# Performance work log

Measured on AMD Instinct MI355X. Metric: run time of the kernel, lower is better.

## Reference

```python
import jax, jax.numpy as jnp
import numpy as np

EPS = 1e-8
WAITK = 9
STRIDE = 1
TARGET_STEP = 0  # module's self.target_step default (training path)
NEG_INF = -1e9


def setup_inputs() -> dict:
    key = jax.random.key(0)
    ks = jax.random.split(key, 5)
    S, B, D, E, H = 2048, 32, 1024, 1024, 1024  # src_len, bsz, dec_dim, enc_dim, energy hidden
    return {
        "input": jax.random.normal(ks[0], (B, D), jnp.float32),
        "source_hids": jax.random.normal(ks[1], (S, B, E), jnp.float32),
        "encoder_padding_mask": jnp.zeros((S, B), dtype=bool),
        "W_dec": jax.random.normal(ks[2], (D, H), jnp.float32) / np.sqrt(D).astype(np.float32),
        "W_enc": jax.random.normal(ks[3], (E, H), jnp.float32) / np.sqrt(E).astype(np.float32),
        "b": jnp.zeros((H,), jnp.float32),
        "v": jax.random.normal(ks[4], (H,), jnp.float32) / np.sqrt(H).astype(np.float32),
    }


def _softattn_energy(inp, source_hids, mask, W_dec, W_enc, b, v):
    # additive energy: v^T tanh(W_dec dec + W_enc enc + b), padding -> -inf
    dec = inp @ W_dec + b                                  # (B, H)
    enc = jnp.einsum('sbe,eh->sbh', source_hids, W_enc)    # (S, B, H)
    e = jnp.einsum('sbh,h->sb', jnp.tanh(enc + dec[None, :, :]), v)  # (S, B)
    return jnp.where(mask, NEG_INF, e)


def reference(input, source_hids, encoder_padding_mask, W_dec, W_enc, b, v):
    S, B, _ = source_hids.shape
    # get_encoder_pointer: min((target_step + waitk - 1 + 1) * stride, src_len - 1)
    ptr = min((TARGET_STEP + WAITK) * STRIDE, S - 1)

    # expected_hard_alignment: one-hot at ptr - 1
    alpha = jnp.zeros((S, B), jnp.float32).at[ptr - 1].set(1.0)

    # expected_soft_alignment: stable exp + eps, zero positions >= ptr, normalize
    e = _softattn_energy(input, source_hids, encoder_padding_mask, W_dec, W_enc, b, v)
    exp_e = jnp.exp(e - jnp.max(e, axis=0, keepdims=True)) + EPS
    keep = (jnp.arange(S) < ptr)[:, None]
    exp_e = jnp.where(keep, exp_e, 0.0)
    beta = exp_e / jnp.sum(exp_e, axis=0, keepdims=True)

    # weighted context: sum_s beta[s,b] * source_hids[s,b,:]
    output = jnp.einsum('sb,sbe->be', beta, source_hids)
    return output, alpha
```

## Files before the change

### kernel.cpp

```cpp
#include <hip/hip_runtime.h>
#include <hip/hip_bf16.h>
#include <math.h>

#define S_LEN 2048
#define B_SZ  32
#define DIM   1024
#define PTR   9
#define EPSV  1e-8f
#define NEGINF -1e9f
#define MROWS 320

typedef __attribute__((ext_vector_type(8)))  short  short8;
typedef __attribute__((ext_vector_type(16))) float  f32x16;

__device__ __forceinline__ short f2bf(float x) {
    __hip_bfloat16 h = __float2bfloat16(x);
    return *(short*)&h;
}

__device__ __forceinline__ float fast_tanh(float x) {
    float xc = fminf(fmaxf(x, -20.f), 20.f);
    float t = __expf(2.f * xc);
    return (t - 1.f) * __builtin_amdgcn_rcpf(t + 1.f);
}

__global__ __launch_bounds__(256) void k_gemm(
    const float* __restrict__ input, const float* __restrict__ src,
    const float* __restrict__ Wdec, const float* __restrict__ Wenc,
    float* __restrict__ Cp, float* __restrict__ alpha)
{
    const int nt = blockIdx.x;
    const int mt = blockIdx.y;
    const int kz = blockIdx.z;
    const float* W     = (mt == 0) ? Wdec : Wenc;
    const float* Abase = (mt == 0) ? input : (src + (size_t)(mt - 1) * B_SZ * DIM);
    const int tid = threadIdx.x;
    const int w = tid >> 6, lane = tid & 63;
    const int r32 = lane & 31, kh = lane >> 5;
    const int kbase = kz * 512 + w * 128;
    const float* Ap = Abase + (size_t)r32 * DIM + kbase + kh * 8;
    const float* Bp = W + (size_t)(kbase + kh * 8) * DIM + nt * 32 + r32;

    if (kz == 0) {
        int bidl = mt * 32 + nt;
        if (bidl < 64) {
            int f = (bidl * 256 + tid) * 4;
            float val = (f >= 256 && f < 288) ? 1.0f : 0.0f;
            float4 o = {val, val, val, val};
            *(float4*)(alpha + f) = o;
        }
    }

    f32x16 acc;
    #pragma unroll
    for (int i = 0; i < 16; i++) acc[i] = 0.f;

    #pragma unroll 4
    for (int k = 0; k < 128; k += 16) {
        float4 a0 = *(const float4*)(Ap + k);
        float4 a1 = *(const float4*)(Ap + k + 4);
        const float* bp = Bp + (size_t)k * DIM;
        float bv0 = bp[0 * DIM], bv1 = bp[1 * DIM], bv2 = bp[2 * DIM], bv3 = bp[3 * DIM];
        float bv4 = bp[4 * DIM], bv5 = bp[5 * DIM], bv6 = bp[6 * DIM], bv7 = bp[7 * DIM];
        short8 af, bf;
        af[0] = f2bf(a0.x); af[1] = f2bf(a0.y); af[2] = f2bf(a0.z); af[3] = f2bf(a0.w);
        af[4] = f2bf(a1.x); af[5] = f2bf(a1.y); af[6] = f2bf(a1.z); af[7] = f2bf(a1.w);
        bf[0] = f2bf(bv0);  bf[1] = f2bf(bv1);  bf[2] = f2bf(bv2);  bf[3] = f2bf(bv3);
        bf[4] = f2bf(bv4);  bf[5] = f2bf(bv5);  bf[6] = f2bf(bv6);  bf[7] = f2bf(bv7);
        acc = __builtin_amdgcn_mfma_f32_32x32x16_bf16(af, bf, acc, 0, 0, 0);
    }

    __shared__ float red[4 * 64 * 17];
    const int base = (w * 64 + lane) * 17;
    #pragma unroll
    for (int r = 0; r < 16; r++) red[base + r] = acc[r];
    __syncthreads();
    const int L = tid & 63, g = tid >> 6;
    const int khL = L >> 5, col = L & 31;
    float* Cz = Cp + (size_t)kz * MROWS * DIM;
    #pragma unroll
    for (int j = 0; j < 4; j++) {
        int r = g * 4 + j;
        float s = red[(0 * 64 + L) * 17 + r] + red[(1 * 64 + L) * 17 + r]
                + red[(2 * 64 + L) * 17 + r] + red[(3 * 64 + L) * 17 + r];
        int row = (r & 3) + 8 * (r >> 2) + 4 * khL;
        Cz[(size_t)(mt * 32 + row) * DIM + nt * 32 + col] = s;
    }
}

__global__ __launch_bounds__(256) void k_tail(
    const float* __restrict__ Cp,
    const unsigned char* __restrict__ mask,
    const float* __restrict__ bias, const float* __restrict__ v,
    const float* __restrict__ src, float* __restrict__ out)
{
    const int b  = blockIdx.x;
    const int hs = blockIdx.y;
    const int tid = threadIdx.x;
    const int h = tid * 4;
    const float* C0 = Cp;
    const float* C1 = Cp + (size_t)MROWS * DIM;

    const int hc = hs * 128 + (tid & 31) * 4;
    float4 sv[PTR];
    #pragma unroll
    for (int s = 0; s < PTR; s++)
        sv[s] = *(const float4*)(src + (size_t)(s * B_SZ + b) * DIM + hc);

    float4 da = *(const float4*)(C0 + (size_t)b * DIM + h);
    float4 db = *(const float4*)(C1 + (size_t)b * DIM + h);
    float4 bb = *(const float4*)(bias + h);
    float4 vv = *(const float4*)(v + h);
    const float bx = da.x + db.x + bb.x, by = da.y + db.y + bb.y,
                bz = da.z + db.z + bb.z, bw = da.w + db.w + bb.w;
    float ps[PTR];
    #pragma unroll
    for (int s = 0; s < PTR; s++) {
        int row = 32 + s * 32 + b;
        float4 e0 = *(const float4*)(C0 + (size_t)row * DIM + h);
        float4 e1 = *(const float4*)(C1 + (size_t)row * DIM + h);
        ps[s] = vv.x * fast_tanh(bx + e0.x + e1.x) + vv.y * fast_tanh(by + e0.y + e1.y)
              + vv.z * fast_tanh(bz + e0.z + e1.z) + vv.w * fast_tanh(bw + e0.w + e1.w);
    }
    __shared__ float red[PTR][4];
    __shared__ float wgt[PTR];
    const int lane = tid & 63, wv = tid >> 6;
    #pragma unroll
    for (int s = 0; s < PTR; s++) {
        float val = ps[s];
        #pragma unroll
        for (int off = 32; off; off >>= 1) val += __shfl_down(val, off);
        if (lane == 0) red[s][wv] = val;
    }
    __syncthreads();
    if (tid == 0) {
        float es[PTR];
        float mx = -INFINITY;
        #pragma unroll
        for (int s = 0; s < PTR; s++) {
            float e = red[s][0] + red[s][1] + red[s][2] + red[s][3];
            if (mask[(size_t)s * B_SZ + b]) e = NEGINF;
            es[s] = e; mx = fmaxf(mx, e);
        }
        float tot = 0.f;
        #pragma unroll
        for (int s = 0; s < PTR; s++) { es[s] = __expf(es[s] - mx) + EPSV; tot += es[s]; }
        float inv = 1.0f / tot;
        #pragma unroll
        for (int s = 0; s < PTR; s++) wgt[s] = es[s] * inv;
    }
    __syncthreads();
    if (tid < 32) {
        float4 acc = {0.f, 0.f, 0.f, 0.f};
        #pragma unroll
        for (int s = 0; s < PTR; s++) {
            float wq = wgt[s];
            acc.x += wq * sv[s].x; acc.y += wq * sv[s].y;
            acc.z += wq * sv[s].z; acc.w += wq * sv[s].w;
        }
        *(float4*)(out + (size_t)b * DIM + hc) = acc;
    }
}

extern "C" void kernel_launch(void* const* d_in, const int* in_sizes, int n_in,
                              void* d_out, int out_size, void* d_ws, size_t ws_size,
                              hipStream_t stream) {
    const float* input = (const float*)d_in[0];
    const float* src   = (const float*)d_in[1];
    const unsigned char* mask = (const unsigned char*)d_in[2];
    const float* Wdec  = (const float*)d_in[3];
    const float* Wenc  = (const float*)d_in[4];
    const float* bias  = (const float*)d_in[5];
    const float* v     = (const float*)d_in[6];
    float* out   = (float*)d_out;
    float* alpha = out + B_SZ * DIM;

    float* Cp = (float*)d_ws;

    k_gemm<<<dim3(32, 10, 2), 256, 0, stream>>>(input, src, Wdec, Wenc, Cp, alpha);
    k_tail<<<dim3(B_SZ, 8), 256, 0, stream>>>(Cp, mask, bias, v, src, out);
}
```

Baseline: 19.76 us.

## Split energy reduction across tail blocks with atomics and raise GEMM split-K

The GEMM split-K factor goes from 2 to 4, so more blocks run with shorter K loops. In the old tail, every block redundantly computed the full 1024-wide energy. Now each block handles only its 128 hidden columns, adds partial energies into a global buffer with atomics, and spin-waits on a per-batch counter until all 8 blocks have contributed. This removes the redundant tanh and reads, but it adds a cross-block busy-wait that depends on all blocks being resident at once, plus extra partial-sum traffic.

```diff
diff --git a/kernel.cpp b/kernel.cpp
--- a/kernel.cpp
+++ b/kernel.cpp
@@ -9,6 +9,7 @@
 #define EPSV  1e-8f
 #define NEGINF -1e9f
 #define MROWS 320
+#define KZ    4
 
 typedef __attribute__((ext_vector_type(8)))  short  short8;
 typedef __attribute__((ext_vector_type(16))) float  f32x16;
@@ -27,7 +28,7 @@
 __global__ __launch_bounds__(256) void k_gemm(
     const float* __restrict__ input, const float* __restrict__ src,
     const float* __restrict__ Wdec, const float* __restrict__ Wenc,
-    float* __restrict__ Cp, float* __restrict__ alpha)
+    float* __restrict__ Cp, float* __restrict__ alpha, unsigned* __restrict__ ezero)
 {
     const int nt = blockIdx.x;
     const int mt = blockIdx.y;
@@ -37,10 +38,13 @@
     const int tid = threadIdx.x;
     const int w = tid >> 6, lane = tid & 63;
     const int r32 = lane & 31, kh = lane >> 5;
-    const int kbase = kz * 512 + w * 128;
+    const int kbase = kz * 256 + w * 64;
     const float* Ap = Abase + (size_t)r32 * DIM + kbase + kh * 8;
     const float* Bp = W + (size_t)(kbase + kh * 8) * DIM + nt * 32 + r32;
 
+    if (nt == 0 && mt == 0 && kz == 0) {
+        for (int i = tid; i < 320; i += 256) ezero[i] = 0u;
+    }
     if (kz == 0) {
         int bidl = mt * 32 + nt;
         if (bidl < 64) {
@@ -55,8 +59,8 @@
     #pragma unroll
     for (int i = 0; i < 16; i++) acc[i] = 0.f;
 
-    #pragma unroll 4
-    for (int k = 0; k < 128; k += 16) {
+    #pragma unroll
+    for (int k = 0; k < 64; k += 16) {
         float4 a0 = *(const float4*)(Ap + k);
         float4 a1 = *(const float4*)(Ap + k + 4);
         const float* bp = Bp + (size_t)k * DIM;
@@ -88,78 +92,81 @@
     }
 }
 
-__global__ __launch_bounds__(256) void k_tail(
+__global__ __launch_bounds__(128) void k_tail(
     const float* __restrict__ Cp,
     const unsigned char* __restrict__ mask,
     const float* __restrict__ bias, const float* __restrict__ v,
-    const float* __restrict__ src, float* __restrict__ out)
+    const float* __restrict__ src, float* __restrict__ out,
+    float* __restrict__ e, unsigned* __restrict__ cnt)
 {
     const int b  = blockIdx.x;
     const int hs = blockIdx.y;
     const int tid = threadIdx.x;
-    const int h = tid * 4;
-    const float* C0 = Cp;
-    const float* C1 = Cp + (size_t)MROWS * DIM;
+    const int col = hs * 128 + tid;
 
-    const int hc = hs * 128 + (tid & 31) * 4;
-    float4 sv[PTR];
+    float sv[PTR];
     #pragma unroll
     for (int s = 0; s < PTR; s++)
-        sv[s] = *(const float4*)(src + (size_t)(s * B_SZ + b) * DIM + hc);
+        sv[s] = src[(size_t)(s * B_SZ + b) * DIM + col];
 
-    float4 da = *(const float4*)(C0 + (size_t)b * DIM + h);
-    float4 db = *(const float4*)(C1 + (size_t)b * DIM + h);
-    float4 bb = *(const float4*)(bias + h);
-    float4 vv = *(const float4*)(v + h);
-    const float bx = da.x + db.x + bb.x, by = da.y + db.y + bb.y,
-                bz = da.z + db.z + bb.z, bw = da.w + db.w + bb.w;
+    float d = bias[col];
+    #pragma unroll
+    for (int p = 0; p < KZ; p++)
+        d += Cp[(size_t)p * MROWS * DIM + (size_t)b * DIM + col];
+    const float vvc = v[col];
+
     float ps[PTR];
     #pragma unroll
     for (int s = 0; s < PTR; s++) {
-        int row = 32 + s * 32 + b;
-        float4 e0 = *(const float4*)(C0 + (size_t)row * DIM + h);
-        float4 e1 = *(const float4*)(C1 + (size_t)row * DIM + h);
-        ps[s] = vv.x * fast_tanh(bx + e0.x + e1.x) + vv.y * fast_tanh(by + e0.y + e1.y)
-              + vv.z * fast_tanh(bz + e0.z + e1.z) + vv.w * fast_tanh(bw + e0.w + e1.w);
+        const int row = 32 + s * 32 + b;
+        float en = 0.f;
+        #pragma unroll
+        for (int p = 0; p < KZ; p++)
+            en += Cp[(size_t)p * MROWS * DIM + (size_t)row * DIM + col];
+        ps[s] = vvc * fast_tanh(d + en);
     }
-    __shared__ float red[PTR][4];
-    __shared__ float wgt[PTR];
-    const int lane = tid & 63, wv = tid >> 6;
+
+    __shared__ float red[PTR][2];
+    __shared__ float lds_e[PTR];
+    const int lane = tid & 63, w = tid >> 6;
     #pragma unroll
     for (int s = 0; s < PTR; s++) {
         float val = ps[s];
         #pragma unroll
         for (int off = 32; off; off >>= 1) val += __shfl_down(val, off);
-        if (lane == 0) red[s][wv] = val;
+        if (lane == 0) red[s][w] = val;
     }
     __syncthreads();
+    if (tid < PTR) atomicAdd(&e[tid * B_SZ + b], red[tid][0] + red[tid][1]);
+    asm volatile("s_waitcnt vmcnt(0)" ::: "memory");
+    __builtin_amdgcn_sched_barrier(0);
+    __syncthreads();
     if (tid == 0) {
-        float es[PTR];
-        float mx = -INFINITY;
-        #pragma unroll
-        for (int s = 0; s < PTR; s++) {
-            float e = red[s][0] + red[s][1] + red[s][2] + red[s][3];
-            if (mask[(size_t)s * B_SZ + b]) e = NEGINF;
-            es[s] = e; mx = fmaxf(mx, e);
+        __hip_atomic_fetch_add(&cnt[b], 1u, __ATOMIC_RELAXED, __HIP_MEMORY_SCOPE_AGENT);
+        int guard = 0;
+        while (__hip_atomic_load(&cnt[b], __ATOMIC_RELAXED, __HIP_MEMORY_SCOPE_AGENT) < 8u) {
+            __builtin_amdgcn_s_sleep(1);
+            if (++guard > (1 << 22)) break;
         }
-        float tot = 0.f;
-        #pragma unroll
-        for (int s = 0; s < PTR; s++) { es[s] = __expf(es[s] - mx) + EPSV; tot += es[s]; }
-        float inv = 1.0f / tot;
-        #pragma unroll
-        for (int s = 0; s < PTR; s++) wgt[s] = es[s] * inv;
     }
     __syncthreads();
-    if (tid < 32) {
-        float4 acc = {0.f, 0.f, 0.f, 0.f};
-        #pragma unroll
-        for (int s = 0; s < PTR; s++) {
-            float wq = wgt[s];
-            acc.x += wq * sv[s].x; acc.y += wq * sv[s].y;
-            acc.z += wq * sv[s].z; acc.w += wq * sv[s].w;
-        }
-        *(float4*)(out + (size_t)b * DIM + hc) = acc;
+    if (tid < PTR) {
+        float ev = __hip_atomic_load(&e[tid * B_SZ + b], __ATOMIC_RELAXED, __HIP_MEMORY_SCOPE_AGENT);
+        if (mask[(size_t)tid * B_SZ + b]) ev = NEGINF;
+        lds_e[tid] = ev;
     }
+    __syncthreads();
+    float es[PTR], mx = -INFINITY;
+    #pragma unroll
+    for (int s = 0; s < PTR; s++) { es[s] = lds_e[s]; mx = fmaxf(mx, es[s]); }
+    float tot = 0.f;
+    #pragma unroll
+    for (int s = 0; s < PTR; s++) { es[s] = __expf(es[s] - mx) + EPSV; tot += es[s]; }
+    const float inv = 1.0f / tot;
+    float acc = 0.f;
+    #pragma unroll
+    for (int s = 0; s < PTR; s++) acc += es[s] * inv * sv[s];
+    out[(size_t)b * DIM + col] = acc;
 }
 
 extern "C" void kernel_launch(void* const* d_in, const int* in_sizes, int n_in,
@@ -176,7 +183,9 @@
     float* alpha = out + B_SZ * DIM;
 
     float* Cp = (float*)d_ws;
+    float* e  = Cp + (size_t)KZ * MROWS * DIM;
+    unsigned* cnt = (unsigned*)(e + 288);
 
-    k_gemm<<<dim3(32, 10, 2), 256, 0, stream>>>(input, src, Wdec, Wenc, Cp, alpha);
-    k_tail<<<dim3(B_SZ, 8), 256, 0, stream>>>(Cp, mask, bias, v, src, out);
+    k_gemm<<<dim3(32, 10, KZ), 256, 0, stream>>>(input, src, Wdec, Wenc, Cp, alpha, (unsigned*)e);
+    k_tail<<<dim3(B_SZ, 8), 128, 0, stream>>>(Cp, mask, bias, v, src, out, e, cnt);
 }
```

New measurement: 25.89 us. 1.31x slower.
